# Kernel tuning notes

Hardware: AMD Instinct MI355X
Metric: run time of the kernel (lower is better)

Reference implementation:

```python
import jax, jax.numpy as jnp
import numpy as np

N, E, D_IN, D_OUT = 100000, 3200000, 128, 128


def setup_inputs() -> dict:
    key = jax.random.key(0)
    ks = jax.random.split(key, 6)
    return {
        "x": jax.random.normal(ks[0], (N, D_IN), dtype=jnp.float32),
        "row": jax.random.randint(ks[1], (E,), 0, N),
        "col": jax.random.randint(ks[2], (E,), 0, N),
        "W0": jax.random.normal(ks[3], (D_OUT, D_IN), dtype=jnp.float32) * (1.0 / np.sqrt(D_IN)),
        "b0": jnp.zeros((D_OUT,), jnp.float32),
        "W1": jax.random.normal(ks[4], (D_OUT, D_IN), dtype=jnp.float32) * (1.0 / np.sqrt(D_IN)),
        "b1": jnp.zeros((D_OUT,), jnp.float32),
        "att": jax.random.normal(ks[5], (2 * D_OUT,), dtype=jnp.float32) * 0.1,
        "scale0": jnp.ones((D_OUT,), jnp.float32),
        "offset0": jnp.zeros((D_OUT,), jnp.float32),
        "scale1": jnp.ones((D_OUT,), jnp.float32),
        "offset1": jnp.zeros((D_OUT,), jnp.float32),
    }


def _norm(f, scale, offset):
    # per-node normalization over feature dim (bias='norm' branch)
    m = jnp.mean(f, axis=1, keepdims=True)
    v = jnp.var(f, axis=1, keepdims=True) + 1e-9
    return (f - m) * scale * jax.lax.rsqrt(v) + offset


def reference(x, row, col, W0, b0, W1, b1, att, scale0, offset0, scale1, offset1):
    d = W0.shape[0]
    # order-0 (self) and order-1 (neighbor) feature transforms, act='relu'
    h0 = jax.nn.relu(x @ W0.T + b0)  # [N, d]
    h1 = jax.nn.relu(x @ W1.T + b1)  # [N, d]
    # unnormalized GAT attention (no softmax), LeakyReLU(0.2)
    a_self = jax.nn.leaky_relu(h0 @ att[:d], negative_slope=0.2)   # [N]
    a_neigh = jax.nn.leaky_relu(h1 @ att[d:], negative_slope=0.2)  # [N]
    e = a_self[row] + a_neigh[col]                                 # [E]
    # SpMM: out[i] = sum_{(i,j) in edges} e_ij * h1[j]
    agg = jax.ops.segment_sum(e[:, None] * h1[col], row, num_segments=h0.shape[0])
    # batch-norm style normalization per head, then mean-aggregate over orders
    out = _norm(h0, scale0, offset0) + _norm(agg, scale1, offset1)
    return out
```

## Files before the change

kernel.cpp:

```cpp
#include <hip/hip_runtime.h>
#include <hip/hip_bf16.h>

constexpr int D = 128;
constexpr int BUCKET_SHIFT = 6;
constexpr int BUCKET_CAP_LOG2 = 12;
constexpr int BUCKET_CAP = 1 << BUCKET_CAP_LOG2;
constexpr int SEG_SHIFT = 13;
constexpr int NSEG = 13;
constexpr int BINS_PER_BUCKET = 4 * NSEG * 16;
constexpr int BINS_PER_WAVE = NSEG * 16;
constexpr int ROWSTRIDE = 130;
typedef __hip_bfloat16 bf16;

__global__ __launch_bounds__(256) void k_gemm(
    const float* __restrict__ x,
    const float* __restrict__ W0, const float* __restrict__ b0,
    const float* __restrict__ W1, const float* __restrict__ b1,
    const float* __restrict__ att,
    float* __restrict__ h0, bf16* __restrict__ h1b,
    float* __restrict__ a_self, float* __restrict__ a_neigh, int N)
{
  constexpr int XS_STRIDE = 132;
  constexpr int WS_STRIDE = 68;
  __shared__ float xs_t[64 * XS_STRIDE];
  __shared__ float ws_t[64 * WS_STRIDE];

  const int t  = threadIdx.x;
  const int nb = blockIdx.x;
  const int fb = blockIdx.y;
  const int n0 = nb * 128;

  const float* __restrict__ W    = (fb < 2) ? W0 : W1;
  const float* __restrict__ bias = (fb < 2) ? b0 : b1;
  float* __restrict__ adest      = (fb < 2) ? a_self : a_neigh;
  const int frow0 = (fb & 1) * 64;

  const int tf = t & 15;
  const int tn = t >> 4;

  const int x_nq = t >> 1;
  const int x_kq = t & 1;
  const int w_f  = t >> 2;
  const int w_kq = t & 3;

  float acc[8][4];
#pragma unroll
  for (int i = 0; i < 8; ++i)
#pragma unroll
    for (int j = 0; j < 4; ++j) acc[i][j] = 0.0f;

  const bool x_ok = (n0 + x_nq) < N;
  const float* xrow = x + (size_t)(n0 + x_nq) * D;
  const float* wrow = W + (size_t)(frow0 + w_f) * D;

  for (int c = 0; c < 2; ++c) {
    const int k0 = c * 64;
    if (c) __syncthreads();

#pragma unroll
    for (int i = 0; i < 8; ++i) {
      const int k = x_kq * 32 + i * 4;
      float4 v = x_ok ? *reinterpret_cast<const float4*>(xrow + k0 + k)
                      : make_float4(0.f, 0.f, 0.f, 0.f);
      xs_t[(k + 0) * XS_STRIDE + x_nq] = v.x;
      xs_t[(k + 1) * XS_STRIDE + x_nq] = v.y;
      xs_t[(k + 2) * XS_STRIDE + x_nq] = v.z;
      xs_t[(k + 3) * XS_STRIDE + x_nq] = v.w;
    }
#pragma unroll
    for (int i = 0; i < 4; ++i) {
      const int k = w_kq * 4 + i * 16;
      float4 v = *reinterpret_cast<const float4*>(wrow + k0 + k);
      ws_t[(k + 0) * WS_STRIDE + w_f] = v.x;
      ws_t[(k + 1) * WS_STRIDE + w_f] = v.y;
      ws_t[(k + 2) * WS_STRIDE + w_f] = v.z;
      ws_t[(k + 3) * WS_STRIDE + w_f] = v.w;
    }
    __syncthreads();

#pragma unroll 4
    for (int k = 0; k < 64; ++k) {
      const float4 a0 = *reinterpret_cast<const float4*>(&xs_t[k * XS_STRIDE + tn * 4]);
      const float4 a1 = *reinterpret_cast<const float4*>(&xs_t[k * XS_STRIDE + 64 + tn * 4]);
      const float4 bvec = *reinterpret_cast<const float4*>(&ws_t[k * WS_STRIDE + tf * 4]);
      const float av[8] = {a0.x, a0.y, a0.z, a0.w, a1.x, a1.y, a1.z, a1.w};
      const float bv[4] = {bvec.x, bvec.y, bvec.z, bvec.w};
#pragma unroll
      for (int i = 0; i < 8; ++i)
#pragma unroll
        for (int j = 0; j < 4; ++j)
          acc[i][j] = fmaf(av[i], bv[j], acc[i][j]);
    }
  }

  const float4 b4 = *reinterpret_cast<const float4*>(&bias[frow0 + tf * 4]);
  const float4 at4 = *reinterpret_cast<const float4*>(
      &att[(fb < 2 ? 0 : 128) + frow0 + tf * 4]);
#pragma unroll
  for (int i = 0; i < 8; ++i) {
    const int nq = (i < 4) ? (tn * 4 + i) : (64 + tn * 4 + (i - 4));
    const int node = n0 + nq;
    float4 r;
    r.x = fmaxf(acc[i][0] + b4.x, 0.0f);
    r.y = fmaxf(acc[i][1] + b4.y, 0.0f);
    r.z = fmaxf(acc[i][2] + b4.z, 0.0f);
    r.w = fmaxf(acc[i][3] + b4.w, 0.0f);
    float pdot = r.x * at4.x + r.y * at4.y + r.z * at4.z + r.w * at4.w;
#pragma unroll
    for (int m2 = 1; m2 < 16; m2 <<= 1) pdot += __shfl_xor(pdot, m2, 16);
    if (node < N) {
      if (fb < 2) {
        *reinterpret_cast<float4*>(&h0[(size_t)node * D + frow0 + tf * 4]) = r;
      } else {
        bf16 p[4] = {__float2bfloat16(r.x), __float2bfloat16(r.y),
                     __float2bfloat16(r.z), __float2bfloat16(r.w)};
        *reinterpret_cast<ushort4*>(&h1b[(size_t)node * D + frow0 + tf * 4]) =
            *reinterpret_cast<const ushort4*>(p);
      }
      if (tf == 0) atomicAdd(&adest[node], pdot);
    }
  }
}

__global__ void k_lrelu(float* __restrict__ a, int n)
{
  int i = blockIdx.x * 256 + threadIdx.x;
  if (i < n) { float v = a[i]; a[i] = v > 0.f ? v : 0.2f * v; }
}

__global__ __launch_bounds__(512) void k_binA(
    const int* __restrict__ row, const int* __restrict__ col,
    int* __restrict__ bukCnt, unsigned* __restrict__ buf1, int E, int NBUK)
{
  constexpr int EPB = 16384;
  __shared__ int hist[1600];
  __shared__ int base[1600];
  const int t = threadIdx.x;
  const int e0 = blockIdx.x * EPB;
  const int e1 = min(e0 + EPB, E);

  for (int i = t; i < NBUK; i += 512) hist[i] = 0;
  __syncthreads();
  for (int e = e0 + t; e < e1; e += 512)
    atomicAdd(&hist[row[e] >> BUCKET_SHIFT], 1);
  __syncthreads();
  for (int bk = t; bk < NBUK; bk += 512) {
    int c = hist[bk];
    base[bk] = (c > 0) ? atomicAdd(&bukCnt[bk], c) : 0;
  }
  __syncthreads();
  for (int i = t; i < NBUK; i += 512) hist[i] = 0;
  __syncthreads();
  for (int e = e0 + t; e < e1; e += 512) {
    int r = row[e];
    int c = col[e];
    int bk = r >> BUCKET_SHIFT;
    int pos = base[bk] + atomicAdd(&hist[bk], 1);
    if (pos < BUCKET_CAP)
      buf1[((size_t)bk << BUCKET_CAP_LOG2) + pos] =
          ((unsigned)c << BUCKET_SHIFT) | (unsigned)(r & 63);
  }
}

__global__ __launch_bounds__(1024) void k_scanB(
    const int* __restrict__ bukCnt, int* __restrict__ bukBase,
    int* __restrict__ runs, int NBUK)
{
  __shared__ int sd[1024];
  __shared__ int carry;
  const int t = threadIdx.x;
  if (t == 0) carry = 0;
  __syncthreads();
  for (int r = 0; r * 1024 < NBUK; ++r) {
    const int idx = r * 1024 + t;
    const int v = (idx < NBUK) ? min(bukCnt[idx], BUCKET_CAP) : 0;
    sd[t] = v;
    __syncthreads();
    for (int d2 = 1; d2 < 1024; d2 <<= 1) {
      int o = (t >= d2) ? sd[t - d2] : 0;
      __syncthreads();
      sd[t] += o;
      __syncthreads();
    }
    const int c0 = carry;
    if (idx < NBUK) bukBase[idx] = c0 + sd[t] - v;
    __syncthreads();
    if (t == 1023) carry = c0 + sd[1023];
    __syncthreads();
  }
  if (t == 0) runs[(size_t)NBUK * BINS_PER_BUCKET] = carry;
}

__global__ __launch_bounds__(256) void k_fine(
    const unsigned* __restrict__ buf1,
    const int* __restrict__ bukCnt, const int* __restrict__ bukBase,
    int* __restrict__ runs, int* __restrict__ colS)
{
  __shared__ int lhist[BINS_PER_BUCKET], labs[BINS_PER_BUCKET], lcur[BINS_PER_BUCKET];
  __shared__ int sd[256];
  const int b = blockIdx.x;
  const int t = threadIdx.x;
  const int n = min(bukCnt[b], BUCKET_CAP);
  const unsigned* src = buf1 + ((size_t)b << BUCKET_CAP_LOG2);

  for (int i = t; i < BINS_PER_BUCKET; i += 256) { lhist[i] = 0; lcur[i] = 0; }
  __syncthreads();
  for (int i = t; i < n; i += 256) {
    unsigned e = src[i];
    int r = e & 63, c = e >> BUCKET_SHIFT;
    int bin = (((r >> 4) * NSEG) + (c >> SEG_SHIFT)) * 16 + (r & 15);
    atomicAdd(&lhist[bin], 1);
  }
  __syncthreads();
  int v[4], s = 0;
  const int bin0 = t * 4;
#pragma unroll
  for (int i = 0; i < 4; ++i) {
    v[i] = (bin0 + i < BINS_PER_BUCKET) ? lhist[bin0 + i] : 0;
    s += v[i];
  }
  sd[t] = s;
  __syncthreads();
  for (int d2 = 1; d2 < 256; d2 <<= 1) {
    int o = (t >= d2) ? sd[t - d2] : 0;
    __syncthreads();
    sd[t] += o;
    __syncthreads();
  }
  int excl = sd[t] - s;
  const int gb = bukBase[b];
#pragma unroll
  for (int i = 0; i < 4; ++i) {
    if (bin0 + i < BINS_PER_BUCKET) {
      labs[bin0 + i] = gb + excl;
      runs[(size_t)b * BINS_PER_BUCKET + bin0 + i] = gb + excl;
    }
    excl += v[i];
  }
  __syncthreads();
  for (int i = t; i < n; i += 256) {
    unsigned e = src[i];
    int r = e & 63, c = e >> BUCKET_SHIFT;
    int bin = (((r >> 4) * NSEG) + (c >> SEG_SHIFT)) * 16 + (r & 15);
    int pos = labs[bin] + atomicAdd(&lcur[bin], 1);
    colS[pos] = (r << 20) | c;
  }
}

__global__ __launch_bounds__(256) void k_agg(
    const float* __restrict__ h0, const bf16* __restrict__ h1b,
    const float* __restrict__ a_self, const float* __restrict__ a_neigh,
    const int* __restrict__ runs, const int* __restrict__ colS,
    const float* __restrict__ scale0, const float* __restrict__ offset0,
    const float* __restrict__ scale1, const float* __restrict__ offset1,
    float* __restrict__ out, int N)
{
  __shared__ float aggL[64 * ROWSTRIDE];
  __shared__ int wb[5];
  __shared__ float asL[64];
  __shared__ int2 je[4][64];
  const int b = blockIdx.x;
  const int t = threadIdx.x;
  const int w = t >> 6, l = t & 63;
  const int rbase = b << 6;

  for (int i = t; i < 64 * ROWSTRIDE; i += 256) aggL[i] = 0.f;
  if (t < 5) wb[t] = runs[(size_t)b * BINS_PER_BUCKET + (size_t)t * BINS_PER_WAVE];
  if (t < 64) {
    float v = (rbase + t < N) ? a_self[rbase + t] : 0.f;
    asL[t] = v > 0.f ? v : 0.2f * v;
  }
  __syncthreads();

  const char* h1c = reinterpret_cast<const char*>(h1b) + l * 4;
  int2* jw = je[w];
  float acc0 = 0.f, acc1 = 0.f;
  int curRow = -1;

  auto flush = [&]() {
    float* pp = &aggL[curRow * ROWSTRIDE + 2 * l];
    const float2 o = *reinterpret_cast<const float2*>(pp);
    *reinterpret_cast<float2*>(pp) = make_float2(o.x + acc0, o.y + acc1);
  };
  auto proc = [&](int2 q, unsigned u) {
    const int r_ = q.x >> 20;
    if (r_ != curRow) {
      if (curRow >= 0) flush();
      acc0 = 0.f; acc1 = 0.f; curRow = r_;
    }
    const float wg = __int_as_float(q.y);
    acc0 = fmaf(wg, __uint_as_float(u << 16), acc0);
    acc1 = fmaf(wg, __uint_as_float(u & 0xffff0000u), acc1);
  };
  auto ld = [&](int2 q) -> unsigned {
    return *reinterpret_cast<const unsigned*>(h1c + ((size_t)(q.x & 0xFFFFF) << 8));
  };

  const int wbeg = wb[w];
  const int wend = wb[w + 1];

  if (wbeg < wend) {
    const int last = wend - 1;
    int P0 = colS[min(wbeg + l, last)];
    float AN0 = a_neigh[P0 & 0xFFFFF];
    int P1 = colS[min(wbeg + 64 + l, last)];

    int cur = wbeg;
    while (cur < wend) {
      const int m = min(64, wend - cur);
      if (l < m) jw[l] = make_int2(P0, __float_as_int(asL[P0 >> 20] + AN0));
      const float ANn = a_neigh[P1 & 0xFFFFF];
      const int Pn = colS[min(cur + 128 + l, last)];

      int k = 0;
      for (; k + 16 <= m; k += 16) {
        int2 q[16]; unsigned u[16];
#pragma unroll
        for (int i = 0; i < 16; ++i) q[i] = jw[k + i];
#pragma unroll
        for (int i = 0; i < 16; ++i) u[i] = ld(q[i]);
#pragma unroll
        for (int i = 0; i < 16; ++i) proc(q[i], u[i]);
      }
      for (; k < m; ++k) {
        const int2 q = jw[k];
        proc(q, ld(q));
      }
      P0 = P1; AN0 = ANn; P1 = Pn;
      cur += m;
    }
    if (curRow >= 0) flush();
  }
  __syncthreads();

  const float2 sc0 = *reinterpret_cast<const float2*>(&scale0[2 * l]);
  const float2 of0 = *reinterpret_cast<const float2*>(&offset0[2 * l]);
  const float2 sc1 = *reinterpret_cast<const float2*>(&scale1[2 * l]);
  const float2 of1 = *reinterpret_cast<const float2*>(&offset1[2 * l]);
  const float inv = 1.0f / 128.0f;
  for (int i = 0; i < 16; ++i) {
    const int node = rbase + (w << 4) + i;
    if (node >= N) break;
    const float2 hv = *reinterpret_cast<const float2*>(&h0[(size_t)node * D + 2 * l]);
    const float2 av = *reinterpret_cast<const float2*>(
        &aggL[((w << 4) + i) * ROWSTRIDE + 2 * l]);
    float sh = hv.x + hv.y, qh = hv.x * hv.x + hv.y * hv.y;
    float sa = av.x + av.y, qa = av.x * av.x + av.y * av.y;
#pragma unroll
    for (int o = 32; o; o >>= 1) {
      sh += __shfl_xor(sh, o, 64); qh += __shfl_xor(qh, o, 64);
      sa += __shfl_xor(sa, o, 64); qa += __shfl_xor(qa, o, 64);
    }
    const float m0 = sh * inv, v0 = qh * inv - m0 * m0 + 1e-9f;
    const float m1 = sa * inv, v1 = qa * inv - m1 * m1 + 1e-9f;
    const float r0 = rsqrtf(v0), r1 = rsqrtf(v1);
    float2 o2;
    o2.x = (hv.x - m0) * sc0.x * r0 + of0.x + (av.x - m1) * sc1.x * r1 + of1.x;
    o2.y = (hv.y - m0) * sc0.y * r0 + of0.y + (av.y - m1) * sc1.y * r1 + of1.y;
    *reinterpret_cast<float2*>(&out[(size_t)node * D + 2 * l]) = o2;
  }
}

extern "C" void kernel_launch(void* const* d_in, const int* in_sizes, int n_in,
                              void* d_out, int out_size, void* d_ws, size_t ws_size,
                              hipStream_t stream)
{
  const float* x       = (const float*)d_in[0];
  const int*   row     = (const int*)d_in[1];
  const int*   col     = (const int*)d_in[2];
  const float* W0      = (const float*)d_in[3];
  const float* b0      = (const float*)d_in[4];
  const float* W1      = (const float*)d_in[5];
  const float* b1      = (const float*)d_in[6];
  const float* att     = (const float*)d_in[7];
  const float* scale0  = (const float*)d_in[8];
  const float* offset0 = (const float*)d_in[9];
  const float* scale1  = (const float*)d_in[10];
  const float* offset1 = (const float*)d_in[11];

  const int N = in_sizes[0] / D;
  const int E = in_sizes[1];
  const int NBUK = (N + 63) >> BUCKET_SHIFT;

  char* ws = (char*)d_ws;
  size_t off = 0;
  auto alloc = [&](size_t bytes) -> void* {
    void* p = ws + off;
    off += (bytes + 511) & ~size_t(511);
    return p;
  };

  float*    h0      = (float*)d_out;
  bf16*     h1b     = (bf16*)alloc((size_t)N * D * sizeof(bf16));
  float*    a_self  = (float*)alloc((size_t)N * sizeof(float));
  float*    a_neigh = (float*)alloc((size_t)N * sizeof(float));
  int*      bukCnt  = (int*)alloc((size_t)NBUK * sizeof(int));
  int*      bukBase = (int*)alloc((size_t)NBUK * sizeof(int));
  int*      runsT   = (int*)alloc(((size_t)NBUK * BINS_PER_BUCKET + 1) * sizeof(int));
  unsigned* buf1    = (unsigned*)alloc(((size_t)NBUK << BUCKET_CAP_LOG2) * sizeof(unsigned));
  int*      colS    = (int*)alloc((size_t)E * sizeof(int));

  hipMemsetAsync(a_self, 0, (size_t)N * sizeof(float), stream);
  hipMemsetAsync(a_neigh, 0, (size_t)N * sizeof(float), stream);
  hipMemsetAsync(bukCnt, 0, (size_t)NBUK * sizeof(int), stream);

  dim3 ggrid((N + 127) / 128, 4);
  k_gemm<<<ggrid, 256, 0, stream>>>(x, W0, b0, W1, b1, att, h0, h1b,
                                    a_self, a_neigh, N);
  const int NBLKA = (E + 16383) / 16384;
  k_binA<<<NBLKA, 512, 0, stream>>>(row, col, bukCnt, buf1, E, NBUK);
  k_scanB<<<1, 1024, 0, stream>>>(bukCnt, bukBase, runsT, NBUK);
  k_fine<<<NBUK, 256, 0, stream>>>(buf1, bukCnt, bukBase, runsT, colS);
  k_lrelu<<<(N + 255) / 256, 256, 0, stream>>>(a_neigh, N);
  k_agg<<<NBUK, 256, 0, stream>>>(h0, h1b, a_self, a_neigh, runsT, colS,
                                  scale0, offset0, scale1, offset1,
                                  (float*)d_out, N);
}
```

Measured before the change: 322.3 us.

## Split aggregation blocks into half-buckets and repack column/row edge encoding

Each 64-row bucket is now handled by two 128-thread blocks of 32 rows each, which doubles the grid and lowers LDS per block so more blocks can be resident. The edge word is repacked so the column sits in the high bits, letting the gather byte offset come from one mask plus the lane offset. Edge metadata is read as int4 pairs. Flushes into shared memory now use atomicAdd, which adds LDS atomic cost. The bank-padded row stride is dropped.

Measured after the change: 1.009 ms. 3.13x slower.

```diff
diff --git a/kernel.cpp b/kernel.cpp
--- a/kernel.cpp
+++ b/kernel.cpp
@@ -9,7 +9,6 @@
 constexpr int NSEG = 13;
 constexpr int BINS_PER_BUCKET = 4 * NSEG * 16;
 constexpr int BINS_PER_WAVE = NSEG * 16;
-constexpr int ROWSTRIDE = 130;
 typedef __hip_bfloat16 bf16;
 
 __global__ __launch_bounds__(256) void k_gemm(
@@ -243,11 +242,11 @@
     int r = e & 63, c = e >> BUCKET_SHIFT;
     int bin = (((r >> 4) * NSEG) + (c >> SEG_SHIFT)) * 16 + (r & 15);
     int pos = labs[bin] + atomicAdd(&lcur[bin], 1);
-    colS[pos] = (r << 20) | c;
-  }
-}
-
-__global__ __launch_bounds__(256) void k_agg(
+    colS[pos] = (int)(((unsigned)c << 8) | (unsigned)r);
+  }
+}
+
+__global__ __launch_bounds__(128, 4) void k_agg(
     const float* __restrict__ h0, const bf16* __restrict__ h1b,
     const float* __restrict__ a_self, const float* __restrict__ a_neigh,
     const int* __restrict__ runs, const int* __restrict__ colS,
@@ -255,76 +254,87 @@
     const float* __restrict__ scale1, const float* __restrict__ offset1,
     float* __restrict__ out, int N)
 {
-  __shared__ float aggL[64 * ROWSTRIDE];
-  __shared__ int wb[5];
-  __shared__ float asL[64];
-  __shared__ int2 je[4][64];
-  const int b = blockIdx.x;
+  __shared__ float aggL[32 * 128];
+  __shared__ int4 je4[2][32];
+  __shared__ float asL[32];
+  __shared__ int wbS[3];
+  const int b2 = blockIdx.x;
+  const int bk = b2 >> 1, h = b2 & 1;
   const int t = threadIdx.x;
   const int w = t >> 6, l = t & 63;
-  const int rbase = b << 6;
-
-  for (int i = t; i < 64 * ROWSTRIDE; i += 256) aggL[i] = 0.f;
-  if (t < 5) wb[t] = runs[(size_t)b * BINS_PER_BUCKET + (size_t)t * BINS_PER_WAVE];
-  if (t < 64) {
+  const int rbase = (bk << 6) + (h << 5);
+
+  for (int i = t; i < 32 * 128; i += 128) aggL[i] = 0.f;
+  if (t < 3)
+    wbS[t] = runs[(size_t)bk * BINS_PER_BUCKET + (size_t)(h * 2 + t) * BINS_PER_WAVE];
+  if (t < 32) {
     float v = (rbase + t < N) ? a_self[rbase + t] : 0.f;
     asL[t] = v > 0.f ? v : 0.2f * v;
   }
   __syncthreads();
 
-  const char* h1c = reinterpret_cast<const char*>(h1b) + l * 4;
-  int2* jw = je[w];
+  const char* __restrict__ h1base = reinterpret_cast<const char*>(h1b);
+  const unsigned l4 = (unsigned)(l * 4);
+  int2* jw = reinterpret_cast<int2*>(je4[w]);
+  const int wbeg = wbS[w], wend = wbS[w + 1];
+
   float acc0 = 0.f, acc1 = 0.f;
   int curRow = -1;
 
   auto flush = [&]() {
-    float* pp = &aggL[curRow * ROWSTRIDE + 2 * l];
-    const float2 o = *reinterpret_cast<const float2*>(pp);
-    *reinterpret_cast<float2*>(pp) = make_float2(o.x + acc0, o.y + acc1);
+    float* pa = &aggL[(curRow << 7) + 2 * l];
+    atomicAdd(pa, acc0);
+    atomicAdd(pa + 1, acc1);
   };
-  auto proc = [&](int2 q, unsigned u) {
-    const int r_ = q.x >> 20;
-    if (r_ != curRow) {
+  auto proc = [&](int qx, int qy, unsigned u) {
+    const int rl = qx & 31;
+    if (rl != curRow) {
       if (curRow >= 0) flush();
-      acc0 = 0.f; acc1 = 0.f; curRow = r_;
-    }
-    const float wg = __int_as_float(q.y);
+      acc0 = 0.f; acc1 = 0.f; curRow = rl;
+    }
+    const float wg = __int_as_float(qy);
     acc0 = fmaf(wg, __uint_as_float(u << 16), acc0);
     acc1 = fmaf(wg, __uint_as_float(u & 0xffff0000u), acc1);
   };
-  auto ld = [&](int2 q) -> unsigned {
-    return *reinterpret_cast<const unsigned*>(h1c + ((size_t)(q.x & 0xFFFFF) << 8));
+  auto gaddr = [&](int qx) -> unsigned {
+    return (((unsigned)qx) & 0xFFFFFF00u) + l4;
   };
-
-  const int wbeg = wb[w];
-  const int wend = wb[w + 1];
 
   if (wbeg < wend) {
     const int last = wend - 1;
     int P0 = colS[min(wbeg + l, last)];
-    float AN0 = a_neigh[P0 & 0xFFFFF];
+    float AN0 = a_neigh[(unsigned)P0 >> 8];
     int P1 = colS[min(wbeg + 64 + l, last)];
 
     int cur = wbeg;
     while (cur < wend) {
       const int m = min(64, wend - cur);
-      if (l < m) jw[l] = make_int2(P0, __float_as_int(asL[P0 >> 20] + AN0));
-      const float ANn = a_neigh[P1 & 0xFFFFF];
+      if (l < m) jw[l] = make_int2(P0, __float_as_int(asL[P0 & 31] + AN0));
+      const float ANn = a_neigh[(unsigned)P1 >> 8];
       const int Pn = colS[min(cur + 128 + l, last)];
 
       int k = 0;
       for (; k + 16 <= m; k += 16) {
-        int2 q[16]; unsigned u[16];
-#pragma unroll
-        for (int i = 0; i < 16; ++i) q[i] = jw[k + i];
-#pragma unroll
-        for (int i = 0; i < 16; ++i) u[i] = ld(q[i]);
-#pragma unroll
-        for (int i = 0; i < 16; ++i) proc(q[i], u[i]);
+        int4 qq[8];
+#pragma unroll
+        for (int i = 0; i < 8; ++i)
+          qq[i] = *reinterpret_cast<const int4*>(&jw[k + 2 * i]);
+        unsigned u[16];
+#pragma unroll
+        for (int i = 0; i < 8; ++i) {
+          u[2 * i]     = *reinterpret_cast<const unsigned*>(h1base + gaddr(qq[i].x));
+          u[2 * i + 1] = *reinterpret_cast<const unsigned*>(h1base + gaddr(qq[i].z));
+        }
+#pragma unroll
+        for (int i = 0; i < 8; ++i) {
+          proc(qq[i].x, qq[i].y, u[2 * i]);
+          proc(qq[i].z, qq[i].w, u[2 * i + 1]);
+        }
       }
       for (; k < m; ++k) {
         const int2 q = jw[k];
-        proc(q, ld(q));
+        const unsigned u = *reinterpret_cast<const unsigned*>(h1base + gaddr(q.x));
+        proc(q.x, q.y, u);
       }
       P0 = P1; AN0 = ANn; P1 = Pn;
       cur += m;
@@ -339,11 +349,11 @@
   const float2 of1 = *reinterpret_cast<const float2*>(&offset1[2 * l]);
   const float inv = 1.0f / 128.0f;
   for (int i = 0; i < 16; ++i) {
-    const int node = rbase + (w << 4) + i;
+    const int rl = (w << 4) + i;
+    const int node = rbase + rl;
     if (node >= N) break;
     const float2 hv = *reinterpret_cast<const float2*>(&h0[(size_t)node * D + 2 * l]);
-    const float2 av = *reinterpret_cast<const float2*>(
-        &aggL[((w << 4) + i) * ROWSTRIDE + 2 * l]);
+    const float2 av = *reinterpret_cast<const float2*>(&aggL[(rl << 7) + 2 * l]);
     float sh = hv.x + hv.y, qh = hv.x * hv.x + hv.y * hv.y;
     float sa = av.x + av.y, qa = av.x * av.x + av.y * av.y;
 #pragma unroll
@@ -412,7 +422,7 @@
   k_scanB<<<1, 1024, 0, stream>>>(bukCnt, bukBase, runsT, NBUK);
   k_fine<<<NBUK, 256, 0, stream>>>(buf1, bukCnt, bukBase, runsT, colS);
   k_lrelu<<<(N + 255) / 256, 256, 0, stream>>>(a_neigh, N);
-  k_agg<<<NBUK, 256, 0, stream>>>(h0, h1b, a_self, a_neigh, runsT, colS,
-                                  scale0, offset0, scale1, offset1,
-                                  (float*)d_out, N);
-}
+  k_agg<<<NBUK * 2, 128, 0, stream>>>(h0, h1b, a_self, a_neigh, runsT, colS,
+                                      scale0, offset0, scale1, offset1,
+                                      (float*)d_out, N);
+}
```

## Precompute edge weights in fine-binning pass and drop lrelu kernel

Applied to the files above, without the earlier changes.

Moves the per-edge attention weight computation (leaky-relu of a_self and a_neigh) into the fine binning kernel, which now writes packed (col<<8|row, weight) int2 records. The standalone lrelu kernel is removed, and the aggregation kernel no longer does a dependent a_neigh gather before each batch of loads. The column is pre-shifted so the byte offset comes straight from the record, and a 4-wide unrolled tail loop is added. In exchange, the sorted edge array doubles in size, adding write and read traffic, and the random a_neigh gather now happens in k_fine.

New measurement: 333.9 us. +3.6%, slower.

```diff
diff --git a/kernel.cpp b/kernel.cpp
--- a/kernel.cpp
+++ b/kernel.cpp
@@ -122,12 +122,6 @@
   }
 }
 
-__global__ void k_lrelu(float* __restrict__ a, int n)
-{
-  int i = blockIdx.x * 256 + threadIdx.x;
-  if (i < n) { float v = a[i]; a[i] = v > 0.f ? v : 0.2f * v; }
-}
-
 __global__ __launch_bounds__(512) void k_binA(
     const int* __restrict__ row, const int* __restrict__ col,
     int* __restrict__ bukCnt, unsigned* __restrict__ buf1, int E, int NBUK)
@@ -194,16 +188,23 @@
 __global__ __launch_bounds__(256) void k_fine(
     const unsigned* __restrict__ buf1,
     const int* __restrict__ bukCnt, const int* __restrict__ bukBase,
-    int* __restrict__ runs, int* __restrict__ colS)
+    const float* __restrict__ a_self, const float* __restrict__ a_neigh,
+    int* __restrict__ runs, int2* __restrict__ colS2, int N)
 {
   __shared__ int lhist[BINS_PER_BUCKET], labs[BINS_PER_BUCKET], lcur[BINS_PER_BUCKET];
+  __shared__ float asF[64];
   __shared__ int sd[256];
   const int b = blockIdx.x;
   const int t = threadIdx.x;
   const int n = min(bukCnt[b], BUCKET_CAP);
   const unsigned* src = buf1 + ((size_t)b << BUCKET_CAP_LOG2);
+  const int rstart = b << BUCKET_SHIFT;
 
   for (int i = t; i < BINS_PER_BUCKET; i += 256) { lhist[i] = 0; lcur[i] = 0; }
+  if (t < 64) {
+    float v = (rstart + t < N) ? a_self[rstart + t] : 0.f;
+    asF[t] = v > 0.f ? v : 0.2f * v;
+  }
   __syncthreads();
   for (int i = t; i < n; i += 256) {
     unsigned e = src[i];
@@ -243,21 +244,21 @@
     int r = e & 63, c = e >> BUCKET_SHIFT;
     int bin = (((r >> 4) * NSEG) + (c >> SEG_SHIFT)) * 16 + (r & 15);
     int pos = labs[bin] + atomicAdd(&lcur[bin], 1);
-    colS[pos] = (r << 20) | c;
+    float an = a_neigh[c];
+    an = an > 0.f ? an : 0.2f * an;
+    colS2[pos] = make_int2((c << 8) | r, __float_as_int(asF[r] + an));
   }
 }
 
 __global__ __launch_bounds__(256) void k_agg(
     const float* __restrict__ h0, const bf16* __restrict__ h1b,
-    const float* __restrict__ a_self, const float* __restrict__ a_neigh,
-    const int* __restrict__ runs, const int* __restrict__ colS,
+    const int* __restrict__ runs, const int2* __restrict__ colS2,
     const float* __restrict__ scale0, const float* __restrict__ offset0,
     const float* __restrict__ scale1, const float* __restrict__ offset1,
     float* __restrict__ out, int N)
 {
   __shared__ float aggL[64 * ROWSTRIDE];
   __shared__ int wb[5];
-  __shared__ float asL[64];
   __shared__ int2 je[4][64];
   const int b = blockIdx.x;
   const int t = threadIdx.x;
@@ -266,10 +267,6 @@
 
   for (int i = t; i < 64 * ROWSTRIDE; i += 256) aggL[i] = 0.f;
   if (t < 5) wb[t] = runs[(size_t)b * BINS_PER_BUCKET + (size_t)t * BINS_PER_WAVE];
-  if (t < 64) {
-    float v = (rbase + t < N) ? a_self[rbase + t] : 0.f;
-    asL[t] = v > 0.f ? v : 0.2f * v;
-  }
   __syncthreads();
 
   const char* h1c = reinterpret_cast<const char*>(h1b) + l * 4;
@@ -283,7 +280,7 @@
     *reinterpret_cast<float2*>(pp) = make_float2(o.x + acc0, o.y + acc1);
   };
   auto proc = [&](int2 q, unsigned u) {
-    const int r_ = q.x >> 20;
+    const int r_ = q.x & 63;
     if (r_ != curRow) {
       if (curRow >= 0) flush();
       acc0 = 0.f; acc1 = 0.f; curRow = r_;
@@ -293,7 +290,8 @@
     acc1 = fmaf(wg, __uint_as_float(u & 0xffff0000u), acc1);
   };
   auto ld = [&](int2 q) -> unsigned {
-    return *reinterpret_cast<const unsigned*>(h1c + ((size_t)(q.x & 0xFFFFF) << 8));
+    return *reinterpret_cast<const unsigned*>(
+        h1c + (size_t)((unsigned)q.x & 0xFFFFFF00u));
   };
 
   const int wbeg = wb[w];
@@ -301,16 +299,13 @@
 
   if (wbeg < wend) {
     const int last = wend - 1;
-    int P0 = colS[min(wbeg + l, last)];
-    float AN0 = a_neigh[P0 & 0xFFFFF];
-    int P1 = colS[min(wbeg + 64 + l, last)];
+    int2 P = colS2[min(wbeg + l, last)];
 
     int cur = wbeg;
     while (cur < wend) {
       const int m = min(64, wend - cur);
-      if (l < m) jw[l] = make_int2(P0, __float_as_int(asL[P0 >> 20] + AN0));
-      const float ANn = a_neigh[P1 & 0xFFFFF];
-      const int Pn = colS[min(cur + 128 + l, last)];
+      if (l < m) jw[l] = P;
+      const int2 Pn = colS2[min(cur + 64 + l, last)];
 
       int k = 0;
       for (; k + 16 <= m; k += 16) {
@@ -321,12 +316,17 @@
         for (int i = 0; i < 16; ++i) u[i] = ld(q[i]);
 #pragma unroll
         for (int i = 0; i < 16; ++i) proc(q[i], u[i]);
+      }
+      for (; k + 4 <= m; k += 4) {
+        const int2 q0 = jw[k], q1 = jw[k + 1], q2 = jw[k + 2], q3 = jw[k + 3];
+        const unsigned u0 = ld(q0), u1 = ld(q1), u2 = ld(q2), u3 = ld(q3);
+        proc(q0, u0); proc(q1, u1); proc(q2, u2); proc(q3, u3);
       }
       for (; k < m; ++k) {
         const int2 q = jw[k];
         proc(q, ld(q));
       }
-      P0 = P1; AN0 = ANn; P1 = Pn;
+      P = Pn;
       cur += m;
     }
     if (curRow >= 0) flush();
@@ -398,7 +398,7 @@
   int*      bukBase = (int*)alloc((size_t)NBUK * sizeof(int));
   int*      runsT   = (int*)alloc(((size_t)NBUK * BINS_PER_BUCKET + 1) * sizeof(int));
   unsigned* buf1    = (unsigned*)alloc(((size_t)NBUK << BUCKET_CAP_LOG2) * sizeof(unsigned));
-  int*      colS    = (int*)alloc((size_t)E * sizeof(int));
+  int2*     colS2   = (int2*)alloc((size_t)E * sizeof(int2));
 
   hipMemsetAsync(a_self, 0, (size_t)N * sizeof(float), stream);
   hipMemsetAsync(a_neigh, 0, (size_t)N * sizeof(float), stream);
@@ -410,9 +410,9 @@
   const int NBLKA = (E + 16383) / 16384;
   k_binA<<<NBLKA, 512, 0, stream>>>(row, col, bukCnt, buf1, E, NBUK);
   k_scanB<<<1, 1024, 0, stream>>>(bukCnt, bukBase, runsT, NBUK);
-  k_fine<<<NBUK, 256, 0, stream>>>(buf1, bukCnt, bukBase, runsT, colS);
-  k_lrelu<<<(N + 255) / 256, 256, 0, stream>>>(a_neigh, N);
-  k_agg<<<NBUK, 256, 0, stream>>>(h0, h1b, a_self, a_neigh, runsT, colS,
+  k_fine<<<NBUK, 256, 0, stream>>>(buf1, bukCnt, bukBase, a_self, a_neigh,
+                                   runsT, colS2, N);
+  k_agg<<<NBUK, 256, 0, stream>>>(h0, h1b, runsT, colS2,
                                   scale0, offset0, scale1, offset1,
                                   (float*)d_out, N);
 }
```
